# Kernel tuning notes

Measured on AMD Instinct MI355X. Metric: run time of the kernel, lower is better.

The kernel has to match this reference:

```python
import jax, jax.numpy as jnp
import numpy as np

H = 2048      # hidden_size
F = 1408      # moe_intermediate_size
E = 8         # num_experts
K = 2         # num_activated_experts
B, S = 4, 1024


def setup_inputs() -> dict:
    key = jax.random.key(0)
    ks = jax.random.split(key, 9)
    sc = 0.02
    return {
        "hidden_states": jax.random.normal(ks[0], (B, S, H), dtype=jnp.float32),
        "gate_w": jax.random.normal(ks[1], (E, H), dtype=jnp.float32) * sc,
        "bias": jnp.zeros((E,), dtype=jnp.float32),
        # shared expert (num_shared_experts = 1); torch Linear weight layout [out, in]
        "ws1": jax.random.normal(ks[2], (F, H), dtype=jnp.float32) * sc,
        "ws2": jax.random.normal(ks[3], (H, F), dtype=jnp.float32) * sc,
        "ws3": jax.random.normal(ks[4], (F, H), dtype=jnp.float32) * sc,
        # routed experts stacked along leading E axis
        "we1": jax.random.normal(ks[5], (E, F, H), dtype=jnp.float32) * sc,
        "we2": jax.random.normal(ks[6], (E, H, F), dtype=jnp.float32) * sc,
        "we3": jax.random.normal(ks[7], (E, F, H), dtype=jnp.float32) * sc,
    }


def reference(hidden_states, gate_w, bias, ws1, ws2, ws3, we1, we2, we3):
    orig_shape = hidden_states.shape
    x = hidden_states.reshape(-1, orig_shape[-1])      # [T, H]
    T = x.shape[0]

    # shared expert (SwiGLU)
    shared = (jax.nn.silu(x @ ws1.T) * (x @ ws3.T)) @ ws2.T   # [T, H]

    # sigmoid gating with bias-adjusted top-k selection
    scores = jax.nn.sigmoid(x @ gate_w.T)              # [T, E]
    routing_scores = scores + bias
    _, topk_idx = jax.lax.top_k(routing_scores, K)     # [T, K]
    sel = jnp.take_along_axis(scores, topk_idx, axis=1)
    gates = sel / sel.sum(axis=-1, keepdims=True)      # [T, K]

    # dense combine weights c[t, e] (top-k indices are distinct per token)
    c = jnp.zeros((T, E), dtype=x.dtype).at[jnp.arange(T)[:, None], topk_idx].add(gates)

    # all-expert SwiGLU, combined with sparse gate weights
    h1 = jnp.einsum("th,efh->etf", x, we1)             # [E, T, F]
    h3 = jnp.einsum("th,efh->etf", x, we3)
    act = jax.nn.silu(h1) * h3
    routed = jnp.einsum("etf,ehf,te->th", act, we2, c) # [T, H]

    return (shared + routed).reshape(orig_shape)
```

## Files before the change

### kernel.cpp

```cpp
#include <hip/hip_runtime.h>
#include <cstdint>
#include <cstddef>

#define TDIM 4096
#define HDIM 2048
#define FDIM 1408
#define NEXP 8
#define NSLOT (TDIM * 2)
#define BK 32

typedef _Float16 half8 __attribute__((ext_vector_type(8)));
typedef _Float16 half4 __attribute__((ext_vector_type(4)));
typedef float floatx4 __attribute__((ext_vector_type(4)));

#define AS1 __attribute__((address_space(1)))
#define AS3 __attribute__((address_space(3)))

__device__ __forceinline__ void g2l16(const _Float16* g, _Float16* l) {
  __builtin_amdgcn_global_load_lds((const AS1 unsigned*)g, (AS3 unsigned*)l, 16, 0, 0);
}

static constexpr size_t ws_align(size_t x) { return (x + 511) & ~(size_t)511; }
static constexpr size_t WS_XB     = 0;
static constexpr size_t WS_ACT_S  = WS_XB    + (size_t)TDIM * HDIM * 2;
static constexpr size_t WS_ACT_R  = WS_ACT_S + (size_t)TDIM * FDIM * 2;
static constexpr size_t WS_TOKE   = WS_ACT_R + (size_t)NSLOT * FDIM * 2;
static constexpr size_t WS_TOKG   = WS_TOKE  + (size_t)TDIM * 2 * 4;
static constexpr size_t WS_SLOTT  = WS_TOKG  + (size_t)TDIM * 2 * 4;
static constexpr size_t WS_SLOTG  = WS_SLOTT + (size_t)NSLOT * 4;
static constexpr size_t WS_COUNTS = WS_SLOTG + (size_t)NSLOT * 4;
static constexpr size_t WS_FILL   = WS_COUNTS + 64;
static constexpr size_t WS_OFFS   = WS_FILL   + 64;
static constexpr size_t WS_WS1H   = ws_align(WS_OFFS + 64);
static constexpr size_t WS_WS3H   = WS_WS1H + (size_t)FDIM * HDIM * 2;
static constexpr size_t WS_WS2H   = WS_WS3H + (size_t)FDIM * HDIM * 2;
static constexpr size_t WS_WE1H   = WS_WS2H + (size_t)HDIM * FDIM * 2;
static constexpr size_t WS_WE3H   = WS_WE1H + (size_t)NEXP * FDIM * HDIM * 2;
static constexpr size_t WS_WE2H   = WS_WE3H + (size_t)NEXP * FDIM * HDIM * 2;
static constexpr size_t WS_END    = WS_WE2H + (size_t)NEXP * HDIM * FDIM * 2;


__global__ void zero_meta_kernel(int* __restrict__ counts) {
  if (threadIdx.x < 32) counts[threadIdx.x] = 0;
}

__global__ void cvt3_kernel(const float* __restrict__ s0, const float* __restrict__ s1,
                            const float* __restrict__ s2, _Float16* __restrict__ d0,
                            _Float16* __restrict__ d1, _Float16* __restrict__ d2) {
  const float* s;
  _Float16* d;
  if (blockIdx.y == 0)      { s = s0; d = d0; }
  else if (blockIdx.y == 1) { s = s1; d = d1; }
  else                      { s = s2; d = d2; }
  size_t i = ((size_t)blockIdx.x * 256 + threadIdx.x) * 8;
  float4 a = *(const float4*)(s + i);
  float4 b = *(const float4*)(s + i + 4);
  half8 h;
  h[0] = (_Float16)a.x; h[1] = (_Float16)a.y; h[2] = (_Float16)a.z; h[3] = (_Float16)a.w;
  h[4] = (_Float16)b.x; h[5] = (_Float16)b.y; h[6] = (_Float16)b.z; h[7] = (_Float16)b.w;
  *(half8*)(d + i) = h;
}

__global__ void gate_kernel(const float* __restrict__ x, const float* __restrict__ gw,
                            const float* __restrict__ bias, _Float16* __restrict__ xb,
                            int* __restrict__ toke, float* __restrict__ tokg,
                            int* __restrict__ counts) {
  const int wid  = blockIdx.x * 4 + (threadIdx.x >> 6);
  const int lane = threadIdx.x & 63;
  const float4* xv = (const float4*)(x + (size_t)wid * HDIM);
  const float4* gv = (const float4*)gw;
  _Float16* xrow = xb + (size_t)wid * HDIM;
  float acc[NEXP];
#pragma unroll
  for (int e = 0; e < NEXP; ++e) acc[e] = 0.f;
#pragma unroll
  for (int i = 0; i < 8; ++i) {
    float4 xq = xv[lane + 64 * i];
    half4 hq;
    hq[0] = (_Float16)xq.x; hq[1] = (_Float16)xq.y;
    hq[2] = (_Float16)xq.z; hq[3] = (_Float16)xq.w;
    *(half4*)(xrow + 4 * (lane + 64 * i)) = hq;
#pragma unroll
    for (int e = 0; e < NEXP; ++e) {
      float4 gq = gv[e * 512 + lane + 64 * i];
      acc[e] += xq.x * gq.x + xq.y * gq.y + xq.z * gq.z + xq.w * gq.w;
    }
  }
#pragma unroll
  for (int e = 0; e < NEXP; ++e) {
    float v = acc[e];
    for (int off = 32; off; off >>= 1) v += __shfl_xor(v, off);
    acc[e] = v;
  }
  if (lane == 0) {
    float s[NEXP], r[NEXP];
#pragma unroll
    for (int e = 0; e < NEXP; ++e) {
      s[e] = 1.f / (1.f + __expf(-acc[e]));
      r[e] = s[e] + bias[e];
    }
    int e0 = 0;
#pragma unroll
    for (int e = 1; e < NEXP; ++e) if (r[e] > r[e0]) e0 = e;
    int e1 = -1;
#pragma unroll
    for (int e = 0; e < NEXP; ++e) if (e != e0 && (e1 < 0 || r[e] > r[e1])) e1 = e;
    float g0 = s[e0], g1 = s[e1];
    float inv = 1.f / (g0 + g1);
    toke[wid * 2]     = e0;
    toke[wid * 2 + 1] = e1;
    tokg[wid * 2]     = g0 * inv;
    tokg[wid * 2 + 1] = g1 * inv;
    atomicAdd(&counts[e0], 1);
    atomicAdd(&counts[e1], 1);
  }
}

__global__ void offsets_kernel(const int* __restrict__ counts, int* __restrict__ offs) {
  if (threadIdx.x == 0) {
    int o = 0;
    for (int e = 0; e < NEXP; ++e) { offs[e] = o; o += counts[e]; }
  }
}

__global__ void scatter_kernel(const int* __restrict__ toke, const float* __restrict__ tokg,
                               const int* __restrict__ offs, int* __restrict__ fill,
                               int* __restrict__ slott, float* __restrict__ slotg) {
  int t = blockIdx.x * 256 + threadIdx.x;
#pragma unroll
  for (int j = 0; j < 2; ++j) {
    int e = toke[t * 2 + j];
    float g = tokg[t * 2 + j];
    int p = offs[e] + atomicAdd(&fill[e], 1);
    slott[p] = t;
    slotg[p] = g;
  }
}


__global__ __launch_bounds__(256) void up_kernel(
    const _Float16* __restrict__ xb,
    const _Float16* __restrict__ ws1h, const _Float16* __restrict__ ws3h,
    const _Float16* __restrict__ we1h, const _Float16* __restrict__ we3h,
    _Float16* __restrict__ acts, _Float16* __restrict__ actr,
    const int* __restrict__ counts, const int* __restrict__ offs,
    const int* __restrict__ slott) {
  const int z = blockIdx.z;
  int cnt = TDIM, base = 0;
  const _Float16* __restrict__ W1 = ws1h;
  const _Float16* __restrict__ W3 = ws3h;
  _Float16* __restrict__ act = acts;
  bool gather = false;
  if (z > 0) {
    const int e = z - 1;
    cnt = counts[e];
    base = offs[e];
    if ((int)(blockIdx.y * 128) >= cnt) return;
    W1 = we1h + (size_t)e * FDIM * HDIM;
    W3 = we3h + (size_t)e * FDIM * HDIM;
    act = actr;
    gather = true;
  }
  const int m0 = blockIdx.y * 128, n0 = blockIdx.x * 128;

  __shared__ _Float16 As[2][128 * BK];
  __shared__ _Float16 B1s[2][128 * BK];
  __shared__ _Float16 B3s[2][128 * BK];

  const int tid = threadIdx.x, lane = tid & 63, wv = tid >> 6;
  const int wm = wv >> 1, wn = wv & 1;
  const int lrow = lane & 15, quad = lane >> 4;

  const _Float16 *srcA[2], *srcB1[2], *srcB3[2];
#pragma unroll
  for (int j = 0; j < 2; ++j) {
    const int rr = wv * 32 + j * 16 + (lane >> 2);
    const int gc = ((lane & 3) ^ ((rr >> 1) & 3)) * 8;
    const int m = m0 + rr;
    int tok;
    if (gather) tok = slott[base + (m < cnt ? m : cnt - 1)];
    else tok = m;
    srcA[j]  = xb + (size_t)tok * HDIM + gc;
    srcB1[j] = W1 + (size_t)(n0 + rr) * HDIM + gc;
    srcB3[j] = W3 + (size_t)(n0 + rr) * HDIM + gc;
  }

  floatx4 acc1[4][4] = {};
  floatx4 acc3[4][4] = {};
  const int cA = (quad ^ ((lrow >> 1) & 3)) * 8;

#pragma unroll
  for (int j = 0; j < 2; ++j) {
    const int lb = (wv * 32 + j * 16) * BK;
    g2l16(srcA[j],  &As[0][lb]);
    g2l16(srcB1[j], &B1s[0][lb]);
    g2l16(srcB3[j], &B3s[0][lb]);
  }
  __syncthreads();

  for (int t = 0; t < HDIM / BK; ++t) {
    const int cur = t & 1;
    if (t + 1 < HDIM / BK) {
      const int k0 = (t + 1) * BK;
#pragma unroll
      for (int j = 0; j < 2; ++j) {
        const int lb = (wv * 32 + j * 16) * BK;
        g2l16(srcA[j] + k0,  &As[cur ^ 1][lb]);
        g2l16(srcB1[j] + k0, &B1s[cur ^ 1][lb]);
        g2l16(srcB3[j] + k0, &B3s[cur ^ 1][lb]);
      }
    }
    half8 af[4], b1f[4], b3f[4];
#pragma unroll
    for (int i = 0; i < 4; ++i)
      af[i] = *(const half8*)&As[cur][(wm * 64 + i * 16 + lrow) * BK + cA];
#pragma unroll
    for (int i = 0; i < 4; ++i) {
      b1f[i] = *(const half8*)&B1s[cur][(wn * 64 + i * 16 + lrow) * BK + cA];
      b3f[i] = *(const half8*)&B3s[cur][(wn * 64 + i * 16 + lrow) * BK + cA];
    }
#pragma unroll
    for (int ms = 0; ms < 4; ++ms)
#pragma unroll
      for (int ns = 0; ns < 4; ++ns) {
        acc1[ms][ns] = __builtin_amdgcn_mfma_f32_16x16x32_f16(af[ms], b1f[ns], acc1[ms][ns], 0, 0, 0);
        acc3[ms][ns] = __builtin_amdgcn_mfma_f32_16x16x32_f16(af[ms], b3f[ns], acc3[ms][ns], 0, 0, 0);
      }
    __syncthreads();
  }

#pragma unroll
  for (int ms = 0; ms < 4; ++ms)
#pragma unroll
    for (int ns = 0; ns < 4; ++ns)
#pragma unroll
      for (int r = 0; r < 4; ++r) {
        float h1 = acc1[ms][ns][r];
        float h3 = acc3[ms][ns][r];
        float a = h1 / (1.f + __expf(-h1)) * h3;
        const int rl = wm * 64 + ms * 16 + quad * 4 + r;
        const int f = n0 + wn * 64 + ns * 16 + lrow;
        const int m = m0 + rl;
        if (gather) {
          if (m < cnt) act[(size_t)(base + m) * FDIM + f] = (_Float16)a;
        } else {
          act[(size_t)m * FDIM + f] = (_Float16)a;
        }
      }
}

__global__ __launch_bounds__(256) void down_kernel(
    const _Float16* __restrict__ acts, const _Float16* __restrict__ actr,
    const _Float16* __restrict__ ws2h, const _Float16* __restrict__ we2h,
    float* __restrict__ out,
    const int* __restrict__ counts, const int* __restrict__ offs,
    const int* __restrict__ slott, const float* __restrict__ slotg) {
  const int z = blockIdx.z;
  int cnt = TDIM, base = 0;
  const _Float16* __restrict__ A = acts;
  const _Float16* __restrict__ W = ws2h;
  bool gather = false;
  if (z > 0) {
    const int e = z - 1;
    cnt = counts[e];
    base = offs[e];
    if ((int)(blockIdx.y * 128) >= cnt) return;
    A = actr;
    W = we2h + (size_t)e * HDIM * FDIM;
    gather = true;
  }
  const int m0 = blockIdx.y * 128, n0 = blockIdx.x * 128;

  __shared__ _Float16 As[2][128 * BK];
  __shared__ _Float16 Bs[2][128 * BK];

  const int tid = threadIdx.x, lane = tid & 63, wv = tid >> 6;
  const int wm = wv >> 1, wn = wv & 1;
  const int lrow = lane & 15, quad = lane >> 4;

  const _Float16 *srcA[2], *srcB[2];
#pragma unroll
  for (int j = 0; j < 2; ++j) {
    const int rr = wv * 32 + j * 16 + (lane >> 2);
    const int gc = ((lane & 3) ^ ((rr >> 1) & 3)) * 8;
    const int m = m0 + rr;
    int srow;
    if (gather) srow = base + (m < cnt ? m : cnt - 1);
    else srow = m;
    srcA[j] = A + (size_t)srow * FDIM + gc;
    srcB[j] = W + (size_t)(n0 + rr) * FDIM + gc;
  }

  floatx4 acc[4][4] = {};
  const int cA = (quad ^ ((lrow >> 1) & 3)) * 8;

#pragma unroll
  for (int j = 0; j < 2; ++j) {
    const int lb = (wv * 32 + j * 16) * BK;
    g2l16(srcA[j], &As[0][lb]);
    g2l16(srcB[j], &Bs[0][lb]);
  }
  __syncthreads();

  for (int t = 0; t < FDIM / BK; ++t) {
    const int cur = t & 1;
    if (t + 1 < FDIM / BK) {
      const int k0 = (t + 1) * BK;
#pragma unroll
      for (int j = 0; j < 2; ++j) {
        const int lb = (wv * 32 + j * 16) * BK;
        g2l16(srcA[j] + k0, &As[cur ^ 1][lb]);
        g2l16(srcB[j] + k0, &Bs[cur ^ 1][lb]);
      }
    }
    half8 af[4], bf[4];
#pragma unroll
    for (int i = 0; i < 4; ++i)
      af[i] = *(const half8*)&As[cur][(wm * 64 + i * 16 + lrow) * BK + cA];
#pragma unroll
    for (int i = 0; i < 4; ++i)
      bf[i] = *(const half8*)&Bs[cur][(wn * 64 + i * 16 + lrow) * BK + cA];
#pragma unroll
    for (int ms = 0; ms < 4; ++ms)
#pragma unroll
      for (int ns = 0; ns < 4; ++ns)
        acc[ms][ns] = __builtin_amdgcn_mfma_f32_16x16x32_f16(af[ms], bf[ns], acc[ms][ns], 0, 0, 0);
    __syncthreads();
  }

#pragma unroll
  for (int ms = 0; ms < 4; ++ms)
#pragma unroll
    for (int ns = 0; ns < 4; ++ns)
#pragma unroll
      for (int r = 0; r < 4; ++r) {
        float v = acc[ms][ns][r];
        const int rl = wm * 64 + ms * 16 + quad * 4 + r;
        const int h = n0 + wn * 64 + ns * 16 + lrow;
        const int m = m0 + rl;
        if (gather) {
          if (m < cnt) {
            const int sl = base + m;
            atomicAdd(&out[(size_t)slott[sl] * HDIM + h], v * slotg[sl]);
          }
        } else {
          atomicAdd(&out[(size_t)m * HDIM + h], v);
        }
      }
}


extern "C" void kernel_launch(void* const* d_in, const int* in_sizes, int n_in,
                              void* d_out, int out_size, void* d_ws, size_t ws_size,
                              hipStream_t stream) {
  const float* x    = (const float*)d_in[0];
  const float* gw   = (const float*)d_in[1];
  const float* bias = (const float*)d_in[2];
  const float* ws1  = (const float*)d_in[3];
  const float* ws2  = (const float*)d_in[4];
  const float* ws3  = (const float*)d_in[5];
  const float* we1  = (const float*)d_in[6];
  const float* we2  = (const float*)d_in[7];
  const float* we3  = (const float*)d_in[8];
  float* out = (float*)d_out;

  char* ws = (char*)d_ws;
  _Float16* xb   = (_Float16*)(ws + WS_XB);
  _Float16* acts = (_Float16*)(ws + WS_ACT_S);
  _Float16* actr = (_Float16*)(ws + WS_ACT_R);
  int*   toke  = (int*)(ws + WS_TOKE);
  float* tokg  = (float*)(ws + WS_TOKG);
  int*   slott = (int*)(ws + WS_SLOTT);
  float* slotg = (float*)(ws + WS_SLOTG);
  int* counts  = (int*)(ws + WS_COUNTS);
  int* fill    = (int*)(ws + WS_FILL);
  int* offs    = (int*)(ws + WS_OFFS);
  _Float16* ws1h = (_Float16*)(ws + WS_WS1H);
  _Float16* ws3h = (_Float16*)(ws + WS_WS3H);
  _Float16* ws2h = (_Float16*)(ws + WS_WS2H);
  _Float16* we1h = (_Float16*)(ws + WS_WE1H);
  _Float16* we3h = (_Float16*)(ws + WS_WE3H);
  _Float16* we2h = (_Float16*)(ws + WS_WE2H);

  hipLaunchKernelGGL(zero_meta_kernel, dim3(1), dim3(64), 0, stream, counts);
  hipLaunchKernelGGL(gate_kernel, dim3(1024), dim3(256), 0, stream, x, gw, bias, xb, toke, tokg, counts);
  hipLaunchKernelGGL(offsets_kernel, dim3(1), dim3(64), 0, stream, counts, offs);
  hipLaunchKernelGGL(scatter_kernel, dim3(16), dim3(256), 0, stream, toke, tokg, offs, fill, slott, slotg);

  constexpr int GS = (FDIM * HDIM) / 2048;
  constexpr int GR = (NEXP * FDIM * HDIM) / 2048;
  hipLaunchKernelGGL(cvt3_kernel, dim3(GS, 3), dim3(256), 0, stream, ws1, ws3, ws2, ws1h, ws3h, ws2h);
  hipLaunchKernelGGL(cvt3_kernel, dim3(GR, 3), dim3(256), 0, stream, we1, we3, we2, we1h, we3h, we2h);

  hipMemsetAsync(out, 0, (size_t)TDIM * HDIM * sizeof(float), stream);

  hipLaunchKernelGGL(up_kernel, dim3(FDIM / 128, TDIM / 128, NEXP + 1), dim3(256), 0, stream,
                     xb, ws1h, ws3h, we1h, we3h, acts, actr, counts, offs, slott);
  hipLaunchKernelGGL(down_kernel, dim3(HDIM / 128, TDIM / 128, NEXP + 1), dim3(256), 0, stream,
                     acts, actr, ws2h, we2h, out, counts, offs, slott, slotg);
}
```

Before: 966.9 us.

## Prefetch two tiles ahead with partial vmcnt waits in both GEMM kernels

Both GEMM main loops now issue global-to-LDS loads for tile t+2 instead of t+1. They wait with s_waitcnt vmcnt(N) so only the older tile must land before use, and __syncthreads is replaced by raw s_barrier pairs. The goal is to keep more memory loads in flight and hide global latency behind MFMA work. In exchange each iteration runs two barriers, and correctness depends on hand-counted vmcnt values matching the loads the compiler actually emits.

Measured after the change: 1.038 ms. +7.3%, slower.

```diff
diff --git a/kernel.cpp b/kernel.cpp
--- a/kernel.cpp
+++ b/kernel.cpp
@@ -19,6 +19,8 @@
 __device__ __forceinline__ void g2l16(const _Float16* g, _Float16* l) {
   __builtin_amdgcn_global_load_lds((const AS1 unsigned*)g, (AS3 unsigned*)l, 16, 0, 0);
 }
+
+#define CFENCE() asm volatile("" ::: "memory")
 
 static constexpr size_t ws_align(size_t x) { return (x + 511) & ~(size_t)511; }
 static constexpr size_t WS_XB     = 0;
@@ -172,6 +174,7 @@
   const int lrow = lane & 15, quad = lane >> 4;
 
   const _Float16 *srcA[2], *srcB1[2], *srcB3[2];
+  int lb_[2];
 #pragma unroll
   for (int j = 0; j < 2; ++j) {
     const int rr = wv * 32 + j * 16 + (lane >> 2);
@@ -183,33 +186,31 @@
     srcA[j]  = xb + (size_t)tok * HDIM + gc;
     srcB1[j] = W1 + (size_t)(n0 + rr) * HDIM + gc;
     srcB3[j] = W3 + (size_t)(n0 + rr) * HDIM + gc;
-  }
+    lb_[j] = (wv * 32 + j * 16) * BK;
+  }
+
+  auto stage = [&](int tt, int b) {
+    const int k0 = tt * BK;
+#pragma unroll
+    for (int j = 0; j < 2; ++j) {
+      g2l16(srcA[j] + k0,  &As[b][lb_[j]]);
+      g2l16(srcB1[j] + k0, &B1s[b][lb_[j]]);
+      g2l16(srcB3[j] + k0, &B3s[b][lb_[j]]);
+    }
+  };
 
   floatx4 acc1[4][4] = {};
   floatx4 acc3[4][4] = {};
   const int cA = (quad ^ ((lrow >> 1) & 3)) * 8;
 
-#pragma unroll
-  for (int j = 0; j < 2; ++j) {
-    const int lb = (wv * 32 + j * 16) * BK;
-    g2l16(srcA[j],  &As[0][lb]);
-    g2l16(srcB1[j], &B1s[0][lb]);
-    g2l16(srcB3[j], &B3s[0][lb]);
-  }
-  __syncthreads();
-
-  for (int t = 0; t < HDIM / BK; ++t) {
-    const int cur = t & 1;
-    if (t + 1 < HDIM / BK) {
-      const int k0 = (t + 1) * BK;
-#pragma unroll
-      for (int j = 0; j < 2; ++j) {
-        const int lb = (wv * 32 + j * 16) * BK;
-        g2l16(srcA[j] + k0,  &As[cur ^ 1][lb]);
-        g2l16(srcB1[j] + k0, &B1s[cur ^ 1][lb]);
-        g2l16(srcB3[j] + k0, &B3s[cur ^ 1][lb]);
-      }
-    }
+  constexpr int NT = HDIM / BK;
+  stage(0, 0);
+  stage(1, 1);
+  asm volatile("s_waitcnt vmcnt(6)" ::: "memory");
+  CFENCE(); __builtin_amdgcn_s_barrier(); CFENCE();
+
+  int cur = 0;
+  for (int t = 0; t < NT; ++t) {
     half8 af[4], b1f[4], b3f[4];
 #pragma unroll
     for (int i = 0; i < 4; ++i)
@@ -226,7 +227,15 @@
         acc1[ms][ns] = __builtin_amdgcn_mfma_f32_16x16x32_f16(af[ms], b1f[ns], acc1[ms][ns], 0, 0, 0);
         acc3[ms][ns] = __builtin_amdgcn_mfma_f32_16x16x32_f16(af[ms], b3f[ns], acc3[ms][ns], 0, 0, 0);
       }
-    __syncthreads();
+    CFENCE(); __builtin_amdgcn_s_barrier(); CFENCE();
+    if (t + 2 < NT) {
+      stage(t + 2, cur);
+      asm volatile("s_waitcnt vmcnt(6)" ::: "memory");
+    } else {
+      asm volatile("s_waitcnt vmcnt(0)" ::: "memory");
+    }
+    CFENCE(); __builtin_amdgcn_s_barrier(); CFENCE();
+    cur ^= 1;
   }
 
 #pragma unroll
@@ -279,6 +288,7 @@
   const int lrow = lane & 15, quad = lane >> 4;
 
   const _Float16 *srcA[2], *srcB[2];
+  int lb_[2];
 #pragma unroll
   for (int j = 0; j < 2; ++j) {
     const int rr = wv * 32 + j * 16 + (lane >> 2);
@@ -289,30 +299,29 @@
     else srow = m;
     srcA[j] = A + (size_t)srow * FDIM + gc;
     srcB[j] = W + (size_t)(n0 + rr) * FDIM + gc;
-  }
+    lb_[j] = (wv * 32 + j * 16) * BK;
+  }
+
+  auto stage = [&](int tt, int b) {
+    const int k0 = tt * BK;
+#pragma unroll
+    for (int j = 0; j < 2; ++j) {
+      g2l16(srcA[j] + k0, &As[b][lb_[j]]);
+      g2l16(srcB[j] + k0, &Bs[b][lb_[j]]);
+    }
+  };
 
   floatx4 acc[4][4] = {};
   const int cA = (quad ^ ((lrow >> 1) & 3)) * 8;
 
-#pragma unroll
-  for (int j = 0; j < 2; ++j) {
-    const int lb = (wv * 32 + j * 16) * BK;
-    g2l16(srcA[j], &As[0][lb]);
-    g2l16(srcB[j], &Bs[0][lb]);
-  }
-  __syncthreads();
-
-  for (int t = 0; t < FDIM / BK; ++t) {
-    const int cur = t & 1;
-    if (t + 1 < FDIM / BK) {
-      const int k0 = (t + 1) * BK;
-#pragma unroll
-      for (int j = 0; j < 2; ++j) {
-        const int lb = (wv * 32 + j * 16) * BK;
-        g2l16(srcA[j] + k0, &As[cur ^ 1][lb]);
-        g2l16(srcB[j] + k0, &Bs[cur ^ 1][lb]);
-      }
-    }
+  constexpr int NT = FDIM / BK;
+  stage(0, 0);
+  stage(1, 1);
+  asm volatile("s_waitcnt vmcnt(4)" ::: "memory");
+  CFENCE(); __builtin_amdgcn_s_barrier(); CFENCE();
+
+  int cur = 0;
+  for (int t = 0; t < NT; ++t) {
     half8 af[4], bf[4];
 #pragma unroll
     for (int i = 0; i < 4; ++i)
@@ -325,7 +334,15 @@
 #pragma unroll
       for (int ns = 0; ns < 4; ++ns)
         acc[ms][ns] = __builtin_amdgcn_mfma_f32_16x16x32_f16(af[ms], bf[ns], acc[ms][ns], 0, 0, 0);
-    __syncthreads();
+    CFENCE(); __builtin_amdgcn_s_barrier(); CFENCE();
+    if (t + 2 < NT) {
+      stage(t + 2, cur);
+      asm volatile("s_waitcnt vmcnt(4)" ::: "memory");
+    } else {
+      asm volatile("s_waitcnt vmcnt(0)" ::: "memory");
+    }
+    CFENCE(); __builtin_amdgcn_s_barrier(); CFENCE();
+    cur ^= 1;
   }
 
 #pragma unroll
```
